# Performance work log

Hardware: AMD Instinct MI355X
Metric: run time of the kernel (lower is better)

## Reference

```python
import jax, jax.numpy as jnp
import numpy as np

B, C, H, W = 64, 512, 32, 32   # batch, channels (=in_dim=model_dim), spatial
N, A = 1, 16                   # n_routers (forced to 1 by the view/matmul shape algebra), num_adapters
EPS = 1e-5                     # torch BatchNorm2d / LayerNorm default eps
INIT_SCALE = 0.02              # config.router_init_scale


def setup_inputs() -> dict:
    key = jax.random.key(0)
    k1, k2 = jax.random.split(key)
    x = jax.random.normal(k1, (B, C, H, W), dtype=jnp.float32)
    router_weights = jax.random.normal(k2, (N, C, A), dtype=jnp.float32) * INIT_SCALE
    router_bias = jnp.zeros((N, A), dtype=jnp.float32)
    bn_gamma = jnp.ones((N, C), dtype=jnp.float32)          # BatchNorm2d weight per router
    bn_beta = jnp.zeros((N, C), dtype=jnp.float32)          # BatchNorm2d bias per router
    ln_gamma = jnp.ones((N, C), dtype=jnp.float32) * INIT_SCALE  # LayerNorm weight (init'd to router_init_scale)
    ln_beta = jnp.zeros((N, C), dtype=jnp.float32)          # LayerNorm bias per router
    return dict(x=x, router_weights=router_weights, router_bias=router_bias,
                bn_gamma=bn_gamma, bn_beta=bn_beta, ln_gamma=ln_gamma, ln_beta=ln_beta)


def reference(x, router_weights, router_bias, bn_gamma, bn_beta, ln_gamma, ln_beta):
    # --- per-router BatchNorm2d (training-mode batch stats over N,H,W) + spatial mean pool ---
    mu = jnp.mean(x, axis=(0, 2, 3))                         # [C]
    var = jnp.var(x, axis=(0, 2, 3))                         # biased, as torch uses for normalization
    xn = (x - mu[None, :, None, None]) * jax.lax.rsqrt(var + EPS)[None, :, None, None]

    def bn_pool(g, b):  # g,b: [C] -> pooled [B,C]
        return jnp.mean(xn * g[None, :, None, None] + b[None, :, None, None], axis=(2, 3))

    new_x = jax.vmap(bn_pool)(bn_gamma, bn_beta)             # [N,B,C]

    # --- normalize_router_weights: LayerNorm over in_dim of router_weights[i].T ---
    wt = jnp.swapaxes(router_weights, 1, 2)                  # [N,A,C]
    m = jnp.mean(wt, axis=-1, keepdims=True)
    v = jnp.var(wt, axis=-1, keepdims=True)
    wn = (wt - m) * jax.lax.rsqrt(v + EPS) * ln_gamma[:, None, :] + ln_beta[:, None, :]
    wn = jnp.swapaxes(wn, 1, 2)                              # [N,C,A]

    # --- routing matmul + bias + softmax (equiv. to view(B,-1) @ W for N=1) ---
    adapter_logits = jnp.einsum('nbc,nca->nba', new_x, wn) + router_bias[:, None, :]  # [N,B,A]
    adapter_probs = jax.nn.softmax(adapter_logits, axis=-1)
    return new_x, adapter_logits, adapter_probs
```

## Files before the change

### kernel.cpp

```cpp
#include <hip/hip_runtime.h>

#define B_DIM 64
#define C_DIM 512
#define A_DIM 16
#define HW    1024
#define EPS   1e-5f

__global__ __launch_bounds__(256) void reduce_rows(const float* __restrict__ x,
                                                   float2* __restrict__ sums) {
    const int wave = threadIdx.x >> 6;
    const int lane = threadIdx.x & 63;
    const int rowA = blockIdx.x * 8 + wave * 2;
    const int rowB = rowA + 1;
    const float4* pA = reinterpret_cast<const float4*>(x) + (size_t)rowA * 256;
    const float4* pB = reinterpret_cast<const float4*>(x) + (size_t)rowB * 256;
    const float4 a0 = pA[lane];
    const float4 a1 = pA[lane + 64];
    const float4 a2 = pA[lane + 128];
    const float4 a3 = pA[lane + 192];
    const float4 b0 = pB[lane];
    const float4 b1 = pB[lane + 64];
    const float4 b2 = pB[lane + 128];
    const float4 b3 = pB[lane + 192];

    float sA = (a0.x + a0.y + a0.z + a0.w) + (a1.x + a1.y + a1.z + a1.w)
             + (a2.x + a2.y + a2.z + a2.w) + (a3.x + a3.y + a3.z + a3.w);
    float qA = (a0.x * a0.x + a0.y * a0.y + a0.z * a0.z + a0.w * a0.w)
             + (a1.x * a1.x + a1.y * a1.y + a1.z * a1.z + a1.w * a1.w)
             + (a2.x * a2.x + a2.y * a2.y + a2.z * a2.z + a2.w * a2.w)
             + (a3.x * a3.x + a3.y * a3.y + a3.z * a3.z + a3.w * a3.w);
    float sB = (b0.x + b0.y + b0.z + b0.w) + (b1.x + b1.y + b1.z + b1.w)
             + (b2.x + b2.y + b2.z + b2.w) + (b3.x + b3.y + b3.z + b3.w);
    float qB = (b0.x * b0.x + b0.y * b0.y + b0.z * b0.z + b0.w * b0.w)
             + (b1.x * b1.x + b1.y * b1.y + b1.z * b1.z + b1.w * b1.w)
             + (b2.x * b2.x + b2.y * b2.y + b2.z * b2.z + b2.w * b2.w)
             + (b3.x * b3.x + b3.y * b3.y + b3.z * b3.z + b3.w * b3.w);

#pragma unroll
    for (int off = 32; off > 0; off >>= 1) {
        sA += __shfl_down(sA, off);
        qA += __shfl_down(qA, off);
        sB += __shfl_down(sB, off);
        qB += __shfl_down(qB, off);
    }
    if (lane == 0) {
        int b = rowA >> 9, c = rowA & (C_DIM - 1);
        sums[c * B_DIM + b] = make_float2(sA, qA);
        b = rowB >> 9;  c = rowB & (C_DIM - 1);
        sums[c * B_DIM + b] = make_float2(sB, qB);
    }
}

__global__ __launch_bounds__(64) void stats_newx_ln(
    const float2* __restrict__ sums,
    const float* __restrict__ bn_g, const float* __restrict__ bn_b,
    const float* __restrict__ rw, const float* __restrict__ ln_g,
    const float* __restrict__ ln_b,
    float* __restrict__ newx, float* __restrict__ wn_t) {
    const int lane = threadIdx.x;
    if (blockIdx.x < C_DIM) {
        const int c = blockIdx.x;
        const float2 t = sums[c * B_DIM + lane];
        float ts = t.x, tq = t.y;
#pragma unroll
        for (int off = 32; off > 0; off >>= 1) {
            ts += __shfl_down(ts, off);
            tq += __shfl_down(tq, off);
        }
        const float mu  = __shfl(ts, 0) * (1.0f / 65536.0f);
        const float var = __shfl(tq, 0) * (1.0f / 65536.0f) - mu * mu;
        const float r   = rsqrtf(var + EPS);
        const float nx  = bn_g[c] * (t.x * (1.0f / 1024.0f) - mu) * r + bn_b[c];
        newx[lane * C_DIM + c] = nx;
    } else {
        const int a = blockIdx.x - C_DIM;
        float wv[8];
        float s = 0.f, q = 0.f;
#pragma unroll
        for (int j = 0; j < 8; j++) {
            const int c = j * 64 + lane;
            wv[j] = rw[c * A_DIM + a];
            s += wv[j];
            q += wv[j] * wv[j];
        }
#pragma unroll
        for (int off = 32; off > 0; off >>= 1) {
            s += __shfl_down(s, off);
            q += __shfl_down(q, off);
        }
        const float m = __shfl(s, 0) * (1.0f / 512.0f);
        const float v = __shfl(q, 0) * (1.0f / 512.0f) - m * m;
        const float r = rsqrtf(v + EPS);
#pragma unroll
        for (int j = 0; j < 8; j++) {
            const int c = j * 64 + lane;
            wn_t[c * A_DIM + a] = (wv[j] - m) * r * ln_g[c] + ln_b[c];
        }
    }
}

__global__ __launch_bounds__(64) void matmul_softmax(
    const float* __restrict__ newx, const float* __restrict__ wn_t,
    const float* __restrict__ rbias,
    float* __restrict__ logits, float* __restrict__ probs) {
    const int b = blockIdx.x;
    const int lane = threadIdx.x;
    const int a = lane & 15;
    const int chunk = lane >> 4;
    const float* xr = newx + b * C_DIM + chunk * 128;
    const float* wr = wn_t + (chunk * 128) * A_DIM + a;
    float acc = 0.f;
#pragma unroll 8
    for (int i = 0; i < 128; i++) {
        acc += xr[i] * wr[i * A_DIM];
    }
    acc += __shfl_xor(acc, 16);
    acc += __shfl_xor(acc, 32);
    const float logit = acc + rbias[a];
    float mx = logit;
#pragma unroll
    for (int m = 1; m < 16; m <<= 1) mx = fmaxf(mx, __shfl_xor(mx, m));
    const float e = expf(logit - mx);
    float se = e;
#pragma unroll
    for (int m = 1; m < 16; m <<= 1) se += __shfl_xor(se, m);
    const float prob = e / se;
    if (lane < 16) {
        logits[b * A_DIM + lane] = logit;
        probs[b * A_DIM + lane] = prob;
    }
}

extern "C" void kernel_launch(void* const* d_in, const int* in_sizes, int n_in,
                              void* d_out, int out_size, void* d_ws, size_t ws_size,
                              hipStream_t stream) {
    const float* x     = (const float*)d_in[0];
    const float* rw    = (const float*)d_in[1];
    const float* rbias = (const float*)d_in[2];
    const float* bn_g  = (const float*)d_in[3];
    const float* bn_b  = (const float*)d_in[4];
    const float* ln_g  = (const float*)d_in[5];
    const float* ln_b  = (const float*)d_in[6];

    float* out    = (float*)d_out;
    float* newx   = out;
    float* logits = out + B_DIM * C_DIM;
    float* probs  = logits + B_DIM * A_DIM;

    float2* sums = (float2*)d_ws;
    float*  wn_t = (float*)(sums + B_DIM * C_DIM);

    reduce_rows<<<(B_DIM * C_DIM) / 8, 256, 0, stream>>>(x, sums);
    stats_newx_ln<<<C_DIM + A_DIM, 64, 0, stream>>>(sums, bn_g, bn_b, rw,
                                                    ln_g, ln_b, newx, wn_t);
    matmul_softmax<<<B_DIM, 64, 0, stream>>>(newx, wn_t, rbias, logits, probs);
}
```

Measured before the change: 206.1 us.

## Fuse BN stats, LayerNorm and routing matmul/softmax into one tail kernel

Merges the stats/newx/LayerNorm kernel and the matmul+softmax kernel into a single 64-block kernel. Each block redundantly recomputes all per-channel BN statistics and the full LayerNorm of the router weights into shared memory, then does its batch row's matmul and softmax. This removes one kernel launch and the global round trip of wn_t, but multiplies the stats work by 64 and serialises 128 channel iterations per wave in few blocks.

```diff
diff --git a/kernel.cpp b/kernel.cpp
--- a/kernel.cpp
+++ b/kernel.cpp
@@ -51,33 +51,45 @@
     }
 }
 
-__global__ __launch_bounds__(64) void stats_newx_ln(
+__global__ __launch_bounds__(256) void fused_tail(
     const float2* __restrict__ sums,
     const float* __restrict__ bn_g, const float* __restrict__ bn_b,
     const float* __restrict__ rw, const float* __restrict__ ln_g,
-    const float* __restrict__ ln_b,
-    float* __restrict__ newx, float* __restrict__ wn_t) {
-    const int lane = threadIdx.x;
-    if (blockIdx.x < C_DIM) {
-        const int c = blockIdx.x;
+    const float* __restrict__ ln_b, const float* __restrict__ rbias,
+    float* __restrict__ newx, float* __restrict__ logits,
+    float* __restrict__ probs) {
+    __shared__ float x_lds[C_DIM];
+    __shared__ float wn_lds[C_DIM * A_DIM];
+    __shared__ float part[4 * A_DIM];
+
+    const int wave = threadIdx.x >> 6;
+    const int lane = threadIdx.x & 63;
+    const int b = blockIdx.x;
+
+    for (int k = 0; k < 128; ++k) {
+        const int c = wave * 128 + k;
         const float2 t = sums[c * B_DIM + lane];
         float ts = t.x, tq = t.y;
 #pragma unroll
         for (int off = 32; off > 0; off >>= 1) {
-            ts += __shfl_down(ts, off);
-            tq += __shfl_down(tq, off);
+            ts += __shfl_xor(ts, off);
+            tq += __shfl_xor(tq, off);
         }
-        const float mu  = __shfl(ts, 0) * (1.0f / 65536.0f);
-        const float var = __shfl(tq, 0) * (1.0f / 65536.0f) - mu * mu;
+        const float mu  = ts * (1.0f / 65536.0f);
+        const float var = tq * (1.0f / 65536.0f) - mu * mu;
         const float r   = rsqrtf(var + EPS);
-        const float nx  = bn_g[c] * (t.x * (1.0f / 1024.0f) - mu) * r + bn_b[c];
-        newx[lane * C_DIM + c] = nx;
-    } else {
-        const int a = blockIdx.x - C_DIM;
+        const float s1b = __shfl(t.x, b);
+        if (lane == 0)
+            x_lds[c] = bn_g[c] * (s1b * (1.0f / 1024.0f) - mu) * r + bn_b[c];
+    }
+
+#pragma unroll
+    for (int i = 0; i < 4; ++i) {
+        const int a = wave * 4 + i;
         float wv[8];
         float s = 0.f, q = 0.f;
 #pragma unroll
-        for (int j = 0; j < 8; j++) {
+        for (int j = 0; j < 8; ++j) {
             const int c = j * 64 + lane;
             wv[j] = rw[c * A_DIM + a];
             s += wv[j];
@@ -85,49 +97,49 @@
         }
 #pragma unroll
         for (int off = 32; off > 0; off >>= 1) {
-            s += __shfl_down(s, off);
-            q += __shfl_down(q, off);
+            s += __shfl_xor(s, off);
+            q += __shfl_xor(q, off);
         }
-        const float m = __shfl(s, 0) * (1.0f / 512.0f);
-        const float v = __shfl(q, 0) * (1.0f / 512.0f) - m * m;
+        const float m = s * (1.0f / 512.0f);
+        const float v = q * (1.0f / 512.0f) - m * m;
         const float r = rsqrtf(v + EPS);
 #pragma unroll
-        for (int j = 0; j < 8; j++) {
+        for (int j = 0; j < 8; ++j) {
             const int c = j * 64 + lane;
-            wn_t[c * A_DIM + a] = (wv[j] - m) * r * ln_g[c] + ln_b[c];
+            wn_lds[c * A_DIM + a] = (wv[j] - m) * r * ln_g[c] + ln_b[c];
         }
     }
-}
+    __syncthreads();
 
-__global__ __launch_bounds__(64) void matmul_softmax(
-    const float* __restrict__ newx, const float* __restrict__ wn_t,
-    const float* __restrict__ rbias,
-    float* __restrict__ logits, float* __restrict__ probs) {
-    const int b = blockIdx.x;
-    const int lane = threadIdx.x;
-    const int a = lane & 15;
-    const int chunk = lane >> 4;
-    const float* xr = newx + b * C_DIM + chunk * 128;
-    const float* wr = wn_t + (chunk * 128) * A_DIM + a;
+    if (threadIdx.x < 128) {
+        reinterpret_cast<float4*>(newx + b * C_DIM)[threadIdx.x] =
+            reinterpret_cast<const float4*>(x_lds)[threadIdx.x];
+    }
+
+    const int a  = lane & 15;
+    const int g  = wave * 4 + (lane >> 4);
     float acc = 0.f;
-#pragma unroll 8
-    for (int i = 0; i < 128; i++) {
-        acc += xr[i] * wr[i * A_DIM];
+#pragma unroll
+    for (int j = 0; j < 32; ++j) {
+        const int c = g * 32 + j;
+        acc += x_lds[c] * wn_lds[c * A_DIM + a];
     }
     acc += __shfl_xor(acc, 16);
     acc += __shfl_xor(acc, 32);
-    const float logit = acc + rbias[a];
-    float mx = logit;
+    if (lane < 16) part[wave * A_DIM + a] = acc;
+    __syncthreads();
+    if (wave == 0 && lane < 16) {
+        const float logit = part[a] + part[A_DIM + a] + part[2 * A_DIM + a]
+                          + part[3 * A_DIM + a] + rbias[a];
+        float mx = logit;
 #pragma unroll
-    for (int m = 1; m < 16; m <<= 1) mx = fmaxf(mx, __shfl_xor(mx, m));
-    const float e = expf(logit - mx);
-    float se = e;
+        for (int m = 1; m < 16; m <<= 1) mx = fmaxf(mx, __shfl_xor(mx, m));
+        const float e = expf(logit - mx);
+        float se = e;
 #pragma unroll
-    for (int m = 1; m < 16; m <<= 1) se += __shfl_xor(se, m);
-    const float prob = e / se;
-    if (lane < 16) {
-        logits[b * A_DIM + lane] = logit;
-        probs[b * A_DIM + lane] = prob;
+        for (int m = 1; m < 16; m <<= 1) se += __shfl_xor(se, m);
+        logits[b * A_DIM + a] = logit;
+        probs[b * A_DIM + a]  = e / se;
     }
 }
 
@@ -148,10 +160,8 @@
     float* probs  = logits + B_DIM * A_DIM;
 
     float2* sums = (float2*)d_ws;
-    float*  wn_t = (float*)(sums + B_DIM * C_DIM);
 
     reduce_rows<<<(B_DIM * C_DIM) / 8, 256, 0, stream>>>(x, sums);
-    stats_newx_ln<<<C_DIM + A_DIM, 64, 0, stream>>>(sums, bn_g, bn_b, rw,
-                                                    ln_g, ln_b, newx, wn_t);
-    matmul_softmax<<<B_DIM, 64, 0, stream>>>(newx, wn_t, rbias, logits, probs);
+    fused_tail<<<B_DIM, 256, 0, stream>>>(sums, bn_g, bn_b, rw, ln_g, ln_b,
+                                          rbias, newx, logits, probs);
 }
```

New measurement: 272.6 us. 32.3% more time.
